# Kernel tuning notes

Measured on AMD Instinct MI355X. Metric: run time of the kernel, lower is better.

The kernel has to match this reference:

```python
import jax, jax.numpy as jnp
import numpy as np

GAMMA = 1.0
BIG = 1e10  # finite stand-in for +inf so gradients stay nan-free


def setup_inputs() -> dict:
    key = jax.random.key(0)
    k1, k2 = jax.random.split(key)
    input_signals = jax.random.normal(k1, (16, 1024), dtype=jnp.float32)  # B x N (equal-length signals)
    ref_signal = jax.random.normal(k2, (1024,), dtype=jnp.float32)        # M
    return {"input_signals": input_signals, "ref_signal": ref_signal}


def _softmin3(a, b, c, gamma):
    z = -jnp.stack([a, b, c], axis=0) / gamma
    return -gamma * jax.nn.logsumexp(z, axis=0)


def _sdtw(D, gamma):
    """Soft-DTW forward DP via anti-diagonal wavefront.
    D: [B, N, M] pairwise squared distances.
    Returns score [B] and padded score matrix R [B, N+1, M+1].
    """
    B, N, M = D.shape
    i_arr = jnp.arange(N + 1)
    # diagonal d holds cells (i, j=d-i); store as vector over i of length N+1
    r0 = jnp.full((B, N + 1), BIG, dtype=D.dtype).at[:, 0].set(0.0)  # d=0: R[0,0]=0
    r1 = jnp.full((B, N + 1), BIG, dtype=D.dtype)                    # d=1: borders = inf

    def shift(x):  # x[:, i] -> x[:, i-1]
        return jnp.concatenate([jnp.full((B, 1), BIG, dtype=x.dtype), x[:, :-1]], axis=1)

    def step(carry, d):
        r_dm2, r_dm1 = carry
        j_arr = d - i_arr
        valid = (i_arr >= 1) & (i_arr <= N) & (j_arr >= 1) & (j_arr <= M)
        i_safe = jnp.clip(i_arr - 1, 0, N - 1)
        j_safe = jnp.clip(j_arr - 1, 0, M - 1)
        Dd = D[:, i_safe, j_safe]  # [B, N+1], D[i-1, j-1] (0-based) = cost at cell (i,j)
        sm = _softmin3(shift(r_dm2), shift(r_dm1), r_dm1, gamma)  # diag, up, left
        rd = jnp.where(valid[None, :], Dd + sm, BIG)
        return (r_dm1, rd), rd

    ds = jnp.arange(2, N + M + 1)
    _, diags = jax.lax.scan(step, (r0, r1), ds)  # [N+M-1, B, N+1]
    full = jnp.concatenate([r0[None], r1[None], diags], axis=0)  # [N+M+1, B, N+1]
    ii, jj = jnp.meshgrid(jnp.arange(N + 1), jnp.arange(M + 1), indexing="ij")
    R = jnp.moveaxis(full[ii + jj, :, ii], -1, 0)  # [B, N+1, M+1]
    score = R[:, N, M]
    return score, R


def reference(input_signals, ref_signal):
    gamma = GAMMA
    # squared-difference cost matrix, B x N x M
    D = (input_signals[:, :, None] - ref_signal[None, None, :]) ** 2
    score, R = _sdtw(D, gamma)
    # gradient matrix E = d(score)/d(D), the soft-DTW alignment matrix
    _, vjp_fn = jax.vjp(lambda Dm: _sdtw(Dm, gamma)[0], D)
    (E,) = vjp_fn(jnp.ones_like(score))
    return score, D, R, E
```

## Files before the change

### kernel.cpp

```cpp
#include <hip/hip_runtime.h>

#define NN 1024
#define MM 1024
#define NB 16
#define BIGF 1.0e10f
#define TP 17
#define NW 8
#define OFS 5
#define CW 16
#define NA 68
#define NGI (OFS * (NW - 1) + NA)

typedef float f32x4 __attribute__((ext_vector_type(4)));

__device__ __forceinline__ float softmin3f(float a, float b, float c) {
  const float mn = fminf(a, fminf(b, c));
  const float mx = fmaxf(a, fmaxf(b, c));
  const float md = __builtin_amdgcn_fmed3f(a, b, c);
  const float s = 1.0f + __expf(mn - md) + __expf(mn - mx);
  return mn - __logf(s);
}

__global__ __launch_bounds__(256) void d_init_kernel(const float* __restrict__ x,
                                                     const float* __restrict__ y,
                                                     float* __restrict__ D) {
  size_t idx = ((size_t)blockIdx.x * blockDim.x + threadIdx.x) * 4;
  int j = (int)(idx & (MM - 1));
  size_t bi = idx >> 10;
  float xi = x[bi];
  const float4 yv = *reinterpret_cast<const float4*>(y + j);
  float t0 = xi - yv.x, t1 = xi - yv.y, t2 = xi - yv.z, t3 = xi - yv.w;
  float4 o;
  o.x = t0 * t0; o.y = t1 * t1; o.z = t2 * t2; o.w = t3 * t3;
  *reinterpret_cast<float4*>(D + idx) = o;
}

__global__ __launch_bounds__(1024) void r_bound_kernel(float* __restrict__ R) {
  int b = blockIdx.x, t = threadIdx.x;
  float* Rb = R + (size_t)b * (NN + 1) * (MM + 1);
  Rb[t + 1] = BIGF;
  Rb[(size_t)(t + 1) * (MM + 1)] = BIGF;
  if (t == 0) Rb[0] = 0.0f;
}

__global__ __launch_bounds__(512) void sdtw_fwd(const float* __restrict__ x,
                                                const float* __restrict__ y,
                                                float* __restrict__ R,
                                                float* __restrict__ score) {
  __shared__ float tile[NW][2112];
  __shared__ float ringR[NW][128];
  const int b = blockIdx.x, t = threadIdx.x;
  const int w = t >> 6, l = t & 63;
  float* __restrict__ Rb = R + (size_t)b * (NN + 1) * (MM + 1);
  const int i1 = 128 * w + 2 * l + 1;
  const float x1 = x[b * NN + i1 - 1];
  const float x2 = x[b * NN + i1];
  float* tl = &tile[w][33 * l];
  const int wm1 = (w > 0) ? (w - 1) : 0;
  const bool L0 = (l == 0), W0 = (w == 0);
  const bool pub = (l == 63) && (w < NW - 1);
  float c1 = BIGF, c2 = BIGF, m1 = BIGF;
  float dgc = BIGF;
  __syncthreads();
  for (int G = 0; G < NGI; ++G) {
    const int a = G - OFS * w;
    if (a >= 0 && a < NA) {
      const int s0 = a * CW;
      float yw[16], rgm[17];
#pragma unroll
      for (int p = 0; p < 16; ++p) {
        const int jy = s0 + p - l - 1;
        yw[p] = y[(jy >= 0 && jy < MM) ? jy : 0];
      }
#pragma unroll
      for (int k = 0; k < 17; ++k) rgm[k] = ringR[wm1][(s0 + k - 1) & 127];
#pragma unroll
      for (int p = 0; p < CW; ++p) {
        const int j = s0 + p - l;
        const bool act = (j >= 1) && (j <= MM);
        const float up_raw = __shfl_up(m1, 1);
        float up = up_raw;
        float dg = dgc;
        if (L0) {
          up = W0 ? BIGF : rgm[p + 1];
          dg = W0 ? ((j == 1) ? 0.0f : BIGF) : ((j == 1) ? BIGF : rgm[p]);
        }
        dgc = up_raw;
        const float yv = yw[p];
        float dv1 = x1 - yv; dv1 *= dv1;
        const float r1 = dv1 + softmin3f(dg, up, c1);
        float dv2 = x2 - yv; dv2 *= dv2;
        const float r2 = dv2 + softmin3f(c1, r1, c2);
        tl[p] = r1;
        tl[16 + p] = r2;
        if (pub && act) ringR[w][j & 127] = r2;
        m1 = act ? r2 : m1;
        c1 = act ? r1 : c1;
        c2 = act ? r2 : c2;
      }
      __builtin_amdgcn_wave_barrier();
#pragma unroll
      for (int g = 0; g < 32; ++g) {
        const int rr = 4 * g + (l >> 4);
        const int sl = l & 15;
        const int col = s0 + sl - (rr >> 1);
        const float v = tile[w][rr * 16 + (rr >> 1) + sl];
        if (col >= 1 && col <= MM)
          Rb[(size_t)(128 * w + 1 + rr) * (MM + 1) + col] = v;
      }
    }
    __syncthreads();
  }
  if (w == NW - 1 && l == 63) score[b] = m1;
}

__global__ __launch_bounds__(1024) void sdtw_bwd(const float* __restrict__ x,
                                                 const float* __restrict__ y,
                                                 const float* __restrict__ R,
                                                 float* __restrict__ E) {
  __shared__ float ypad[3088];
  __shared__ float rbx[4][NN + 2];
  __shared__ float ebx[4][NN + 2];
  __shared__ float tile[NN][TP];
  const int b = blockIdx.x, t = threadIdx.x;
  const int i = t + 1;
  const float* __restrict__ Rb = R + (size_t)b * (NN + 1) * (MM + 1);
  float* __restrict__ Eb = E + (size_t)b * (size_t)NN * MM;
  for (int k = t; k < 3088; k += 1024)
    ypad[k] = (k >= 1025 && k < 1025 + MM) ? y[k - 1025] : 0.0f;
#pragma unroll
  for (int q = 0; q < 4; ++q) { rbx[q][i] = -BIGF; ebx[q][i] = 0.0f; }
  if (t == NN - 1) {
#pragma unroll
    for (int q = 0; q < 4; ++q) { rbx[q][NN + 1] = -BIGF; ebx[q][NN + 1] = 0.0f; }
  }
  const float xi = x[b * NN + t];
  const float xi1 = x[b * NN + ((t + 1 < NN) ? (t + 1) : t)];
  const bool seedrow = (i == NN);
  float rt_e = 0.0f, rt_r = -BIGF;
  float dgn_e = 0.0f, dgn_r = -BIGF;
#pragma unroll
  for (int pass = 0; pass < 4; ++pass) {
    const int row = (pass << 8) + (t >> 2);
    const int ir = row + 1;
    const int c4 = (t & 3) << 2;
    const int jb2 = (128 << 4) - ir + c4;
    if (jb2 >= 1 && jb2 + 3 <= MM) {
      const float4 v = *reinterpret_cast<const float4*>(Rb + (size_t)ir * (MM + 1) + jb2);
      tile[row][c4] = v.x; tile[row][c4 + 1] = v.y;
      tile[row][c4 + 2] = v.z; tile[row][c4 + 3] = v.w;
    } else {
#pragma unroll
      for (int c = 0; c < 4; ++c) {
        const int jc = jb2 + c;
        tile[row][c4 + c] =
            (jc >= 1 && jc <= MM) ? Rb[(size_t)ir * (MM + 1) + jc] : -BIGF;
      }
    }
  }
  __syncthreads();
  float yj = ypad[3088 - i];

  for (int K = 128; K >= 0; --K) {
    const int d0 = K << 4;
#pragma unroll
    for (int p = 0; p < 16; ++p) {
      const int s = 15 - p;
      const int d = d0 + s;
      const int j = d - i;
      const bool act = (j >= 1) && (j <= MM);
      const float dn_r = rbx[(s + 1) & 3][i + 1];
      const float dn_e = ebx[(s + 1) & 3][i + 1];
      const float yjm1 = ypad[j + 1024];
      const float rij = tile[t][s];
      float d1 = xi1 - yjm1; d1 *= d1;
      float d2 = xi - yj;    d2 *= d2;
      float d3 = xi1 - yj;   d3 *= d3;
      const float a1 = dn_r - rij - d1;
      const float a2 = rt_r - rij - d2;
      const float a3 = dgn_r - rij - d3;
      float acc = dn_e * __expf(a1) + rt_e * __expf(a2) + dgn_e * __expf(a3);
      if (seedrow && j == MM) acc += 1.0f;
      rbx[s & 3][i] = act ? rij : -BIGF;
      ebx[s & 3][i] = act ? acc : 0.0f;
      tile[t][s] = act ? acc : 0.0f;
      rt_e = act ? acc : 0.0f;
      rt_r = act ? rij : -BIGF;
      dgn_e = dn_e; dgn_r = dn_r;
      yj = yjm1;
      __syncthreads();
    }
#pragma unroll
    for (int pass = 0; pass < 4; ++pass) {
      const int row = (pass << 8) + (t >> 2);
      const int ir = row + 1;
      const int c4 = (t & 3) << 2;
      const int jb2 = d0 - ir + c4;
      float fv[4];
#pragma unroll
      for (int c = 0; c < 4; ++c) fv[c] = tile[row][c4 + c];
      if (jb2 >= 1 && jb2 + 3 <= MM) {
        f32x4 v;
        v[0] = fv[0]; v[1] = fv[1]; v[2] = fv[2]; v[3] = fv[3];
        const float* pp = Eb + (size_t)row * MM + (jb2 - 1);
        asm volatile("global_store_dwordx4 %0, %1, off" ::"v"(pp), "v"(v) : "memory");
      } else if (jb2 + 3 >= 1 && jb2 <= MM) {
#pragma unroll
        for (int c = 0; c < 4; ++c) {
          const int jc = jb2 + c;
          if (jc >= 1 && jc <= MM) Eb[(size_t)row * MM + (jc - 1)] = fv[c];
        }
      }
      const int jn = jb2 - 16;
      if (jn >= 1 && jn + 3 <= MM) {
        const float4 v = *reinterpret_cast<const float4*>(Rb + (size_t)ir * (MM + 1) + jn);
        tile[row][c4] = v.x; tile[row][c4 + 1] = v.y;
        tile[row][c4 + 2] = v.z; tile[row][c4 + 3] = v.w;
      } else {
#pragma unroll
        for (int c = 0; c < 4; ++c) {
          const int jc = jn + c;
          tile[row][c4 + c] =
              (jc >= 1 && jc <= MM) ? Rb[(size_t)ir * (MM + 1) + jc] : -BIGF;
        }
      }
    }
    __syncthreads();
  }
}

extern "C" void kernel_launch(void* const* d_in, const int* in_sizes, int n_in,
                              void* d_out, int out_size, void* d_ws, size_t ws_size,
                              hipStream_t stream) {
  const float* x = (const float*)d_in[0];
  const float* y = (const float*)d_in[1];
  float* out = (float*)d_out;
  float* score = out;
  float* D = out + NB;
  float* R = D + (size_t)NB * NN * MM;
  float* E = R + (size_t)NB * (NN + 1) * (MM + 1);

  hipLaunchKernelGGL(d_init_kernel, dim3((NB * NN * MM) / (256 * 4)), dim3(256), 0, stream,
                     x, y, D);
  hipLaunchKernelGGL(r_bound_kernel, dim3(NB), dim3(1024), 0, stream, R);
  hipLaunchKernelGGL(sdtw_fwd, dim3(NB), dim3(512), 0, stream, x, y, R, score);
  hipLaunchKernelGGL(sdtw_bwd, dim3(NB), dim3(1024), 0, stream, x, y, R, E);
}
```

Baseline: 1.372 ms.

## Restructure soft-DTW backward as wave-per-row-band wavefront with shuffles

The backward kernel no longer runs one thread per row with a block-wide barrier on every anti-diagonal step. Each of 16 wavefronts now owns a 64-row band and processes 16-column chunks, offset in time from the next band (skewed wavefront). Within a wave, values pass between rows by lane shuffles, and across bands through shared-memory ring buffers, so there is one block barrier per chunk instead of one per diagonal. This trades far fewer barriers for pipeline fill/drain steps, per-lane global loads of y, and scalar rather than vectorised E stores and R loads.

```diff
diff --git a/kernel.cpp b/kernel.cpp
--- a/kernel.cpp
+++ b/kernel.cpp
@@ -4,12 +4,15 @@
 #define MM 1024
 #define NB 16
 #define BIGF 1.0e10f
-#define TP 17
 #define NW 8
 #define OFS 5
 #define CW 16
 #define NA 68
 #define NGI (OFS * (NW - 1) + NA)
+#define BW 16
+#define BOFS 5
+#define BNA 68
+#define BNGI (BOFS * (BW - 1) + BNA)
 
 typedef float f32x4 __attribute__((ext_vector_type(4)));
 
@@ -118,112 +121,95 @@
                                                  const float* __restrict__ y,
                                                  const float* __restrict__ R,
                                                  float* __restrict__ E) {
-  __shared__ float ypad[3088];
-  __shared__ float rbx[4][NN + 2];
-  __shared__ float ebx[4][NN + 2];
-  __shared__ float tile[NN][TP];
+  __shared__ float tile[BW][1088];
+  __shared__ float ringE[BW + 1][128];
+  __shared__ float ringR[BW + 1][128];
   const int b = blockIdx.x, t = threadIdx.x;
-  const int i = t + 1;
+  const int k = t >> 6, l = t & 63;
   const float* __restrict__ Rb = R + (size_t)b * (NN + 1) * (MM + 1);
   float* __restrict__ Eb = E + (size_t)b * (size_t)NN * MM;
-  for (int k = t; k < 3088; k += 1024)
-    ypad[k] = (k >= 1025 && k < 1025 + MM) ? y[k - 1025] : 0.0f;
-#pragma unroll
-  for (int q = 0; q < 4; ++q) { rbx[q][i] = -BIGF; ebx[q][i] = 0.0f; }
-  if (t == NN - 1) {
-#pragma unroll
-    for (int q = 0; q < 4; ++q) { rbx[q][NN + 1] = -BIGF; ebx[q][NN + 1] = 0.0f; }
-  }
-  const float xi = x[b * NN + t];
-  const float xi1 = x[b * NN + ((t + 1 < NN) ? (t + 1) : t)];
-  const bool seedrow = (i == NN);
-  float rt_e = 0.0f, rt_r = -BIGF;
-  float dgn_e = 0.0f, dgn_r = -BIGF;
-#pragma unroll
-  for (int pass = 0; pass < 4; ++pass) {
-    const int row = (pass << 8) + (t >> 2);
-    const int ir = row + 1;
-    const int c4 = (t & 3) << 2;
-    const int jb2 = (128 << 4) - ir + c4;
-    if (jb2 >= 1 && jb2 + 3 <= MM) {
-      const float4 v = *reinterpret_cast<const float4*>(Rb + (size_t)ir * (MM + 1) + jb2);
-      tile[row][c4] = v.x; tile[row][c4 + 1] = v.y;
-      tile[row][c4 + 2] = v.z; tile[row][c4 + 3] = v.w;
-    } else {
-#pragma unroll
-      for (int c = 0; c < 4; ++c) {
-        const int jc = jb2 + c;
-        tile[row][c4 + c] =
-            (jc >= 1 && jc <= MM) ? Rb[(size_t)ir * (MM + 1) + jc] : -BIGF;
-      }
-    }
-  }
+  const int i = 64 * k + l + 1;
+  const float xi = x[b * NN + i - 1];
+  const float xi1 = x[b * NN + ((i < NN) ? i : (NN - 1))];
+  for (int q = t; q < (BW + 1) * 128; q += 1024) {
+    (&ringE[0][0])[q] = 0.0f;
+    (&ringR[0][0])[q] = -BIGF;
+  }
+  const bool L63 = (l == 63);
+  const bool seedlane = (i == NN);
+  float pE = 0.f, pR = -BIGF;
+  float gE = 0.f, gR = -BIGF;
+  float* tl = &tile[k][17 * l];
   __syncthreads();
-  float yj = ypad[3088 - i];
-
-  for (int K = 128; K >= 0; --K) {
-    const int d0 = K << 4;
-#pragma unroll
-    for (int p = 0; p < 16; ++p) {
-      const int s = 15 - p;
-      const int d = d0 + s;
-      const int j = d - i;
-      const bool act = (j >= 1) && (j <= MM);
-      const float dn_r = rbx[(s + 1) & 3][i + 1];
-      const float dn_e = ebx[(s + 1) & 3][i + 1];
-      const float yjm1 = ypad[j + 1024];
-      const float rij = tile[t][s];
-      float d1 = xi1 - yjm1; d1 *= d1;
-      float d2 = xi - yj;    d2 *= d2;
-      float d3 = xi1 - yj;   d3 *= d3;
-      const float a1 = dn_r - rij - d1;
-      const float a2 = rt_r - rij - d2;
-      const float a3 = dgn_r - rij - d3;
-      float acc = dn_e * __expf(a1) + rt_e * __expf(a2) + dgn_e * __expf(a3);
-      if (seedrow && j == MM) acc += 1.0f;
-      rbx[s & 3][i] = act ? rij : -BIGF;
-      ebx[s & 3][i] = act ? acc : 0.0f;
-      tile[t][s] = act ? acc : 0.0f;
-      rt_e = act ? acc : 0.0f;
-      rt_r = act ? rij : -BIGF;
-      dgn_e = dn_e; dgn_r = dn_r;
-      yj = yjm1;
-      __syncthreads();
-    }
-#pragma unroll
-    for (int pass = 0; pass < 4; ++pass) {
-      const int row = (pass << 8) + (t >> 2);
-      const int ir = row + 1;
-      const int c4 = (t & 3) << 2;
-      const int jb2 = d0 - ir + c4;
-      float fv[4];
-#pragma unroll
-      for (int c = 0; c < 4; ++c) fv[c] = tile[row][c4 + c];
-      if (jb2 >= 1 && jb2 + 3 <= MM) {
-        f32x4 v;
-        v[0] = fv[0]; v[1] = fv[1]; v[2] = fv[2]; v[3] = fv[3];
-        const float* pp = Eb + (size_t)row * MM + (jb2 - 1);
-        asm volatile("global_store_dwordx4 %0, %1, off" ::"v"(pp), "v"(v) : "memory");
-      } else if (jb2 + 3 >= 1 && jb2 <= MM) {
-#pragma unroll
-        for (int c = 0; c < 4; ++c) {
-          const int jc = jb2 + c;
-          if (jc >= 1 && jc <= MM) Eb[(size_t)row * MM + (jc - 1)] = fv[c];
-        }
-      }
-      const int jn = jb2 - 16;
-      if (jn >= 1 && jn + 3 <= MM) {
-        const float4 v = *reinterpret_cast<const float4*>(Rb + (size_t)ir * (MM + 1) + jn);
-        tile[row][c4] = v.x; tile[row][c4 + 1] = v.y;
-        tile[row][c4 + 2] = v.z; tile[row][c4 + 3] = v.w;
-      } else {
-#pragma unroll
-        for (int c = 0; c < 4; ++c) {
-          const int jc = jn + c;
-          tile[row][c4 + c] =
-              (jc >= 1 && jc <= MM) ? Rb[(size_t)ir * (MM + 1) + jc] : -BIGF;
-        }
-      }
+#pragma unroll
+  for (int g = 0; g < 16; ++g) {
+    const int rr = 4 * g + (l >> 4);
+    const int c16 = l & 15;
+    const int col = 1087 - rr - 15 + c16;
+    tile[k][17 * rr + 15 - c16] =
+        (col >= 1 && col <= MM) ? Rb[(size_t)(64 * k + 1 + rr) * (MM + 1) + col] : BIGF;
+  }
+  if (l < 16) ringR[k][(1087 - l) & 127] = tile[k][l];
+  __syncthreads();
+
+  for (int C = 0; C < BNGI; ++C) {
+    const int a = C - (BW - 1 - k) * BOFS;
+    if (a >= 0 && a < BNA) {
+      const int J0w = 1087 - 16 * a;
+      const int J0 = J0w - l;
+      float yw[16];
+#pragma unroll
+      for (int s = 0; s < 16; ++s) {
+        const int jy = J0 - s - 1;
+        yw[s] = (jy >= 0 && jy < MM) ? y[jy] : 0.0f;
+      }
+      float yj = (J0 >= 0 && J0 < MM) ? y[J0] : 0.0f;
+      float rgE_[17], rgR_[17];
+#pragma unroll
+      for (int u = 0; u < 17; ++u) {
+        const int cu = (1025 - 16 * a - u) & 127;
+        rgE_[u] = ringE[k + 1][cu];
+        rgR_[u] = ringR[k + 1][cu];
+      }
+#pragma unroll
+      for (int s = 0; s < 16; ++s) {
+        const int j = J0 - s;
+        const bool act = (j >= 1) && (j <= MM);
+        float dnE = __shfl_down(pE, 1);
+        float dnR = __shfl_down(pR, 1);
+        if (L63) { dnE = rgE_[s + 1]; dnR = rgR_[s + 1]; }
+        const float dgE = gE, dgR = gR;
+        const float rij = tl[s];
+        const float yjm = yw[s];
+        float d1 = xi1 - yjm; d1 *= d1;
+        float d2 = xi - yj;   d2 *= d2;
+        float d3 = xi1 - yj;  d3 *= d3;
+        float e = dnE * __expf(dnR - rij - d1) + pE * __expf(pR - rij - d2) +
+                  dgE * __expf(dgR - rij - d3);
+        if (seedlane && j == MM) e += 1.0f;
+        tl[s] = e;
+        gE = dnE; gR = dnR;
+        pE = act ? e : pE;
+        pR = act ? rij : pR;
+        yj = yjm;
+      }
+      __builtin_amdgcn_wave_barrier();
+      if (l < 16) ringE[k][(J0w - l) & 127] = tile[k][l];
+#pragma unroll
+      for (int g = 0; g < 16; ++g) {
+        const int rr = 4 * g + (l >> 4);
+        const int c16 = l & 15;
+        const int ad = 17 * rr + 15 - c16;
+        const int col = J0w - rr - 15 + c16;
+        const float ev = tile[k][ad];
+        if (col >= 1 && col <= MM)
+          Eb[(size_t)(64 * k + rr) * MM + (col - 1)] = ev;
+        const int colN = col - 16;
+        tile[k][ad] = (colN >= 1 && colN <= MM)
+                          ? Rb[(size_t)(64 * k + 1 + rr) * (MM + 1) + colN]
+                          : BIGF;
+      }
+      if (l < 16) ringR[k][(J0w - 16 - l) & 127] = tile[k][l];
     }
     __syncthreads();
   }
```

Result: slower. 1.904 ms (+38.8%).
